# Performance work log

Hardware: AMD Instinct MI355X
Metric: run time of the kernel (lower is better)

The kernel has to match this reference:

```python
import jax, jax.numpy as jnp
import numpy as np

N_NODES = 50000
N_EDGES = 800000
IN_FEAT = 128
HIDDEN = 128
HEADS = 4
HEAD_DIM = HIDDEN // HEADS  # 32
N_LAYERS = 3
N_GRAPHS = 64
NEG_SLOPE = 0.2
LN_EPS = 1e-5


def setup_inputs() -> dict:
    key = jax.random.key(0)
    ks = jax.random.split(key, 12)
    x = jax.random.normal(ks[0], (N_NODES, IN_FEAT), dtype=jnp.float32)
    edge_index = jax.random.randint(ks[1], (2, N_EDGES), 0, N_NODES, dtype=jnp.int64)
    batch = jnp.sort(jax.random.randint(ks[2], (N_NODES,), 0, N_GRAPHS, dtype=jnp.int64))
    s = 0.05
    emb_W = jax.random.normal(ks[3], (IN_FEAT, HIDDEN), dtype=jnp.float32) * s
    emb_b = jnp.zeros((HIDDEN,), dtype=jnp.float32)
    lin_l_W = jax.random.normal(ks[4], (N_LAYERS, HIDDEN, HIDDEN), dtype=jnp.float32) * s
    lin_l_b = jnp.zeros((N_LAYERS, HIDDEN), dtype=jnp.float32)
    lin_r_W = jax.random.normal(ks[5], (N_LAYERS, HIDDEN, HIDDEN), dtype=jnp.float32) * s
    lin_r_b = jnp.zeros((N_LAYERS, HIDDEN), dtype=jnp.float32)
    att = jax.random.normal(ks[6], (N_LAYERS, HEADS, HEAD_DIM), dtype=jnp.float32) * s
    conv_b = jnp.zeros((N_LAYERS, HIDDEN), dtype=jnp.float32)
    ln_g = jnp.ones((N_LAYERS, HIDDEN), dtype=jnp.float32)
    ln_b = jnp.zeros((N_LAYERS, HIDDEN), dtype=jnp.float32)
    return {"x": x, "edge_index": edge_index, "batch": batch,
            "emb_W": emb_W, "emb_b": emb_b,
            "lin_l_W": lin_l_W, "lin_l_b": lin_l_b,
            "lin_r_W": lin_r_W, "lin_r_b": lin_r_b,
            "att": att, "conv_b": conv_b, "ln_g": ln_g, "ln_b": ln_b}


def _gatv2_layer(x, src, dst, Wl, bl, Wr, br, att_w, bias):
    # x: [N, HIDDEN]; src/dst: [E]; att_w: [H, C]
    N = x.shape[0]
    xl = (x @ Wl + bl).reshape(N, HEADS, HEAD_DIM)  # source transform
    xr = (x @ Wr + br).reshape(N, HEADS, HEAD_DIM)  # target transform
    e = jax.nn.leaky_relu(xl[src] + xr[dst], NEG_SLOPE)      # [E, H, C]
    logits = jnp.einsum('ehc,hc->eh', e, att_w)              # [E, H]
    # segment softmax over edges grouped by destination node
    seg_max = jax.ops.segment_max(logits, dst, num_segments=N)  # [N, H]
    seg_max = jnp.where(jnp.isfinite(seg_max), seg_max, 0.0)
    ex = jnp.exp(logits - seg_max[dst])
    denom = jax.ops.segment_sum(ex, dst, num_segments=N)
    alpha = ex / (denom[dst] + 1e-16)                        # [E, H]
    msg = alpha[..., None] * xl[src]                         # [E, H, C]
    out = jax.ops.segment_sum(msg, dst, num_segments=N)      # [N, H, C]
    return out.reshape(N, HIDDEN) + bias


def _layer_norm(x, g, b):
    mu = jnp.mean(x, axis=-1, keepdims=True)
    var = jnp.mean(jnp.square(x - mu), axis=-1, keepdims=True)
    return (x - mu) * jax.lax.rsqrt(var + LN_EPS) * g + b


def reference(x, edge_index, batch, emb_W, emb_b, lin_l_W, lin_l_b,
              lin_r_W, lin_r_b, att, conv_b, ln_g, ln_b):
    src, dst = edge_index[0], edge_index[1]
    h = x @ emb_W + emb_b
    for l in range(N_LAYERS):
        res = h
        h = _gatv2_layer(h, src, dst, lin_l_W[l], lin_l_b[l],
                         lin_r_W[l], lin_r_b[l], att[l], conv_b[l])
        h = jax.nn.elu(h)          # dropout in eval mode = identity
        h = h + res
        h = _layer_norm(h, ln_g[l], ln_b[l])
    # global mean pool over graphs
    sums = jax.ops.segment_sum(h, batch, num_segments=N_GRAPHS)
    counts = jax.ops.segment_sum(jnp.ones((h.shape[0], 1), h.dtype), batch,
                                 num_segments=N_GRAPHS)
    return sums / jnp.maximum(counts, 1.0)
```

## Files before the change

### kernel.cpp

```cpp
#include <hip/hip_runtime.h>
#include <hip/hip_bf16.h>
#include <math.h>


#define HID 128
#define BKT_SHIFT 7
#define BKT_DSTS (1 << BKT_SHIFT)
#define CAP_SHIFT 12
#define CAP (1 << CAP_SHIFT)

typedef __attribute__((ext_vector_type(8))) short bf8_t;
typedef __attribute__((ext_vector_type(8))) _Float16 hf8_t;
typedef __attribute__((ext_vector_type(2))) _Float16 h2_t;
typedef __attribute__((ext_vector_type(4))) float f4_t;

__device__ __forceinline__ unsigned short f2bf(float f) {
    unsigned u = __float_as_uint(f);
    u += 0x7fff + ((u >> 16) & 1);
    return (unsigned short)(u >> 16);
}
__device__ __forceinline__ float bf2f(unsigned short h) {
    return __uint_as_float(((unsigned)h) << 16);
}
__device__ __forceinline__ unsigned short f2h(float f) {
    _Float16 h = (_Float16)f;
    return __builtin_bit_cast(unsigned short, h);
}
__device__ __forceinline__ float h2f(unsigned short u) {
    return (float)__builtin_bit_cast(_Float16, u);
}
__device__ __forceinline__ h2_t shfl_xor_h2(h2_t v, int m) {
    return __builtin_bit_cast(h2_t, __shfl_xor(__builtin_bit_cast(int, v), m, 64));
}


__global__ __launch_bounds__(256) void bin_edges(const int* __restrict__ ei,
                                                 int* __restrict__ bucketCursor,
                                                 int* __restrict__ tmp,
                                                 int E, int NBK, int perBlk) {
    extern __shared__ int sh[];
    int* hist = sh;
    int* base = sh + NBK;
    int tid = threadIdx.x;
    int e0 = blockIdx.x * perBlk;
    int e1 = e0 + perBlk; if (e1 > E) e1 = E;

    for (int b = tid; b < NBK; b += 256) hist[b] = 0;
    __syncthreads();
    for (int e = e0 + tid; e < e1; e += 256)
        atomicAdd(&hist[ei[E + e] >> BKT_SHIFT], 1);
    __syncthreads();
    for (int b = tid; b < NBK; b += 256) {
        int c = hist[b];
        if (c > 0) base[b] = atomicAdd(&bucketCursor[b], c);
        hist[b] = 0;
    }
    __syncthreads();
    for (int e = e0 + tid; e < e1; e += 256) {
        int d = ei[E + e];
        int b = d >> BKT_SHIFT;
        int pos = (b << CAP_SHIFT) + base[b] + atomicAdd(&hist[b], 1);
        tmp[pos] = ei[e] | ((d & (BKT_DSTS - 1)) << 16);
    }
}

__global__ __launch_bounds__(256) void bucket_build(const int* __restrict__ tmp,
                                                    const int* __restrict__ bucketCursor,
                                                    int* __restrict__ offsets,
                                                    int* __restrict__ deg,
                                                    unsigned short* __restrict__ srt,
                                                    int N) {
    __shared__ int hist[BKT_DSTS];
    __shared__ int cur[BKT_DSTS];
    int b = blockIdx.x;
    int d0 = b << BKT_SHIFT;
    int tid = threadIdx.x;
    if (tid < BKT_DSTS) hist[tid] = 0;
    __syncthreads();
    int start = b << CAP_SHIFT;
    int end = start + bucketCursor[b];
    for (int i = start + tid; i < end; i += 256)
        atomicAdd(&hist[(tmp[i] >> 16) & (BKT_DSTS - 1)], 1);
    __syncthreads();
    int v = (tid < BKT_DSTS) ? hist[tid] : 0;
    if (tid < BKT_DSTS) cur[tid] = v;
    __syncthreads();
    for (int off = 1; off < BKT_DSTS; off <<= 1) {
        int u = (tid < BKT_DSTS && tid >= off) ? cur[tid - off] : 0;
        __syncthreads();
        if (tid < BKT_DSTS) cur[tid] += u;
        __syncthreads();
    }
    if (tid < BKT_DSTS) {
        int ex = start + cur[tid] - v;
        int d = d0 + tid;
        if (d < N) { offsets[d] = ex; deg[d] = v; }
        cur[tid] = ex;
    }
    __syncthreads();
    for (int i = start + tid; i < end; i += 256) {
        int r = tmp[i];
        int pos = atomicAdd(&cur[(r >> 16) & (BKT_DSTS - 1)], 1);
        srt[pos] = (unsigned short)(r & 0xFFFF);
    }
}

__global__ __launch_bounds__(256) void prep_wfrag_all(const float* __restrict__ embW,
                                                      const float* __restrict__ linlW,
                                                      const float* __restrict__ linrW,
                                                      unsigned short* __restrict__ frag) {
    int w = blockIdx.y;
    const float* W;
    if (w == 0)      W = embW;
    else if (w <= 3) W = linlW + (size_t)(w - 1) * 16384;
    else             W = linrW + (size_t)(w - 4) * 16384;

    int i = blockIdx.x * 256 + threadIdx.x;
    int j = i & 7;
    int lane = (i >> 3) & 63;
    int t = i >> 9;
    int kk = t >> 3, nn = t & 7;
    int k = kk * 32 + (lane >> 4) * 8 + j;
    int n = nn * 16 + (lane & 15);
    float v = W[k * 128 + n];
    if (w == 0) {
        unsigned short hi = f2bf(v);
        frag[i] = hi;
        frag[16384 + i] = f2bf(v - bf2f(hi));
    } else {
        int slot = (w <= 3) ? (1 + 2 * (w - 1)) : (2 + 2 * (w - 4));
        frag[32768 + (size_t)(slot - 1) * 16384 + i] = f2h(v);
    }
}


__global__ __launch_bounds__(256) void gemm_emb(
    const float* __restrict__ Afp,
    const unsigned short* __restrict__ Bf,
    const float* __restrict__ bias,
    unsigned short* __restrict__ Chi, unsigned short* __restrict__ Clo, int M) {
    __shared__ __align__(16) unsigned short As[2][64][136];
    int m0 = blockIdx.x * 64;
    int tid = threadIdx.x;

    #pragma unroll
    for (int i = 0; i < 8; ++i) {
        int idx = tid + i * 256;
        int r = idx >> 5, c4 = idx & 31;
        int row = m0 + r;
        float4 v = make_float4(0.f, 0.f, 0.f, 0.f);
        if (row < M) v = *(const float4*)(Afp + (size_t)row * HID + c4 * 4);
        ushort4 hi, lo;
        hi.x = f2bf(v.x); lo.x = f2bf(v.x - bf2f(hi.x));
        hi.y = f2bf(v.y); lo.y = f2bf(v.y - bf2f(hi.y));
        hi.z = f2bf(v.z); lo.z = f2bf(v.z - bf2f(hi.z));
        hi.w = f2bf(v.w); lo.w = f2bf(v.w - bf2f(hi.w));
        *(ushort4*)&As[0][r][c4 * 4] = hi;
        *(ushort4*)&As[1][r][c4 * 4] = lo;
    }
    __syncthreads();

    int wave = tid >> 6, lane = tid & 63;
    int mrow = lane & 15;
    int quad = lane >> 4;

    f4_t acc[8];
    #pragma unroll
    for (int nn = 0; nn < 8; ++nn) acc[nn] = (f4_t)(0.f);

    #pragma unroll
    for (int kk = 0; kk < 4; ++kk) {
        bf8_t ah = *(const bf8_t*)&As[0][wave * 16 + mrow][kk * 32 + quad * 8];
        bf8_t al = *(const bf8_t*)&As[1][wave * 16 + mrow][kk * 32 + quad * 8];
        const unsigned short* bp = Bf + kk * 4096 + lane * 8;
        #pragma unroll
        for (int nn = 0; nn < 8; ++nn) {
            bf8_t bh = *(const bf8_t*)(bp + nn * 512);
            bf8_t bl = *(const bf8_t*)(bp + nn * 512 + 16384);
            acc[nn] = __builtin_amdgcn_mfma_f32_16x16x32_bf16(ah, bh, acc[nn], 0, 0, 0);
            acc[nn] = __builtin_amdgcn_mfma_f32_16x16x32_bf16(ah, bl, acc[nn], 0, 0, 0);
            acc[nn] = __builtin_amdgcn_mfma_f32_16x16x32_bf16(al, bh, acc[nn], 0, 0, 0);
        }
    }

    int lrow0 = wave * 16 + quad * 4;
    __syncthreads();
    #pragma unroll
    for (int nn = 0; nn < 8; ++nn) {
        int col = nn * 16 + mrow;
        float b = bias[col];
        #pragma unroll
        for (int r = 0; r < 4; ++r) {
            float o = acc[nn][r] + b;
            unsigned short hh = f2h(o);
            As[0][lrow0 + r][col] = hh;
            As[1][lrow0 + r][col] = f2h(o - h2f(hh));
        }
    }
    __syncthreads();
    #pragma unroll
    for (int i = 0; i < 4; ++i) {
        int idx = tid + i * 256;
        int r = idx >> 4, c8 = idx & 15;
        int row = m0 + r;
        if (row < M) {
            *(uint4*)(Chi + (size_t)row * HID + c8 * 8) = *(uint4*)&As[0][r][c8 * 8];
            *(uint4*)(Clo + (size_t)row * HID + c8 * 8) = *(uint4*)&As[1][r][c8 * 8];
        }
    }
}


__global__ __launch_bounds__(256) void gemm_dual_f16(
    const unsigned short* __restrict__ Ah,
    const unsigned short* __restrict__ Bf0, const unsigned short* __restrict__ Bf1,
    const float* __restrict__ b0, const float* __restrict__ b1,
    unsigned short* __restrict__ C0h, unsigned short* __restrict__ C1h, int M) {
    __shared__ __align__(16) unsigned short As[2][64][136];
    int m0 = blockIdx.x * 64;
    int tid = threadIdx.x;

    #pragma unroll
    for (int i = 0; i < 4; ++i) {
        int idx = tid + i * 256;
        int r = idx >> 4, c8 = idx & 15;
        int row = m0 + r;
        uint4 v = make_uint4(0, 0, 0, 0);
        if (row < M) v = *(const uint4*)(Ah + (size_t)row * HID + c8 * 8);
        *(uint4*)&As[0][r][c8 * 8] = v;
    }
    __syncthreads();

    int wave = tid >> 6, lane = tid & 63;
    int mrow = lane & 15;
    int quad = lane >> 4;

    f4_t acc0[8], acc1[8];
    #pragma unroll
    for (int nn = 0; nn < 8; ++nn) {
        acc0[nn] = (f4_t)(0.f);
        acc1[nn] = (f4_t)(0.f);
    }

    #pragma unroll
    for (int kk = 0; kk < 4; ++kk) {
        hf8_t a = *(const hf8_t*)&As[0][wave * 16 + mrow][kk * 32 + quad * 8];
        const unsigned short* bp0 = Bf0 + kk * 4096 + lane * 8;
        const unsigned short* bp1 = Bf1 + kk * 4096 + lane * 8;
        #pragma unroll
        for (int nn = 0; nn < 8; ++nn) {
            hf8_t bb0 = *(const hf8_t*)(bp0 + nn * 512);
            hf8_t bb1 = *(const hf8_t*)(bp1 + nn * 512);
            acc0[nn] = __builtin_amdgcn_mfma_f32_16x16x32_f16(a, bb0, acc0[nn], 0, 0, 0);
            acc1[nn] = __builtin_amdgcn_mfma_f32_16x16x32_f16(a, bb1, acc1[nn], 0, 0, 0);
        }
    }

    int lrow0 = wave * 16 + quad * 4;
    __syncthreads();
    #pragma unroll
    for (int nn = 0; nn < 8; ++nn) {
        int col = nn * 16 + mrow;
        float bb0 = b0[col];
        float bb1 = b1[col];
        #pragma unroll
        for (int r = 0; r < 4; ++r) {
            As[0][lrow0 + r][col] = f2h(acc0[nn][r] + bb0);
            As[1][lrow0 + r][col] = f2h(acc1[nn][r] + bb1);
        }
    }
    __syncthreads();
    #pragma unroll
    for (int i = 0; i < 4; ++i) {
        int idx = tid + i * 256;
        int r = idx >> 4, c8 = idx & 15;
        int row = m0 + r;
        if (row < M) {
            *(uint4*)(C0h + (size_t)row * HID + c8 * 8) = *(uint4*)&As[0][r][c8 * 8];
            *(uint4*)(C1h + (size_t)row * HID + c8 * 8) = *(uint4*)&As[1][r][c8 * 8];
        }
    }
}


__device__ __forceinline__ void edge_math(uint4 rv, const h2_t xr2[4], const h2_t av2[4],
                                          h2_t xv[4], float* pOut) {
    const h2_t slope2 = {(_Float16)0.2f, (_Float16)0.2f};
    xv[0] = __builtin_bit_cast(h2_t, rv.x); xv[1] = __builtin_bit_cast(h2_t, rv.y);
    xv[2] = __builtin_bit_cast(h2_t, rv.z); xv[3] = __builtin_bit_cast(h2_t, rv.w);
    h2_t p2 = (h2_t)((_Float16)0.f);
    #pragma unroll
    for (int i = 0; i < 4; ++i) {
        h2_t e = xv[i] + xr2[i];
        e = __builtin_elementwise_max(e, e * slope2);
        p2 = e * av2[i] + p2;
    }
    *pOut = (float)p2[0] + (float)p2[1];
}

__global__ __launch_bounds__(256) void gat_layer(
    const unsigned short* __restrict__ xlh,
    const unsigned short* __restrict__ xrh,
    const int* __restrict__ offsets, const int* __restrict__ deg,
    const unsigned short* __restrict__ srt,
    const float* __restrict__ att,
    const float* __restrict__ convb,
    const float* __restrict__ lng, const float* __restrict__ lnb,
    unsigned short* __restrict__ Hhi, unsigned short* __restrict__ Hlo, int N) {
    int wv = (blockIdx.x * blockDim.x + threadIdx.x) >> 6;
    int lane = threadIdx.x & 63;
    if (wv >= N) return;
    int n = wv;
    int quarter = lane >> 4;
    int f0 = (lane & 15) * 8;
    const unsigned short* xbase = xlh + f0;

    h2_t xr2[4], av2[4];
    {
        uint4 xv = *(const uint4*)(xrh + (size_t)n * HID + f0);
        xr2[0] = __builtin_bit_cast(h2_t, xv.x);
        xr2[1] = __builtin_bit_cast(h2_t, xv.y);
        xr2[2] = __builtin_bit_cast(h2_t, xv.z);
        xr2[3] = __builtin_bit_cast(h2_t, xv.w);
        float a[8];
        *(float4*)&a[0] = *(const float4*)(att + f0);
        *(float4*)&a[4] = *(const float4*)(att + f0 + 4);
        #pragma unroll
        for (int i = 0; i < 4; ++i)
            av2[i] = (h2_t){(_Float16)a[2 * i], (_Float16)a[2 * i + 1]};
    }

    float d = 0.f;
    h2_t acc2[4];
    #pragma unroll
    for (int i = 0; i < 4; ++i) acc2[i] = (h2_t)((_Float16)0.f);
    int start = offsets[n], cnt = deg[n];

    int j = 0;
    for (; j + 16 <= cnt; j += 16) {
        int s[4];
        #pragma unroll
        for (int u = 0; u < 4; ++u) s[u] = srt[start + j + 4 * u + quarter];
        uint4 rv[4];
        #pragma unroll
        for (int u = 0; u < 4; ++u)
            rv[u] = *(const uint4*)(xbase + (size_t)s[u] * HID);
        h2_t xv[4][4];
        float p[4];
        #pragma unroll
        for (int u = 0; u < 4; ++u) edge_math(rv[u], xr2, av2, xv[u], &p[u]);
        h2_t p01 = {(_Float16)p[0], (_Float16)p[1]};
        h2_t p23 = {(_Float16)p[2], (_Float16)p[3]};
        p01 += shfl_xor_h2(p01, 1); p23 += shfl_xor_h2(p23, 1);
        p01 += shfl_xor_h2(p01, 2); p23 += shfl_xor_h2(p23, 2);
        float w[4];
        w[0] = __expf((float)p01[0]); w[1] = __expf((float)p01[1]);
        w[2] = __expf((float)p23[0]); w[3] = __expf((float)p23[1]);
        #pragma unroll
        for (int u = 0; u < 4; ++u) {
            d += w[u];
            h2_t w2 = (h2_t)((_Float16)w[u]);
            #pragma unroll
            for (int i = 0; i < 4; ++i) acc2[i] = w2 * xv[u][i] + acc2[i];
        }
    }
    for (; j + 4 <= cnt; j += 4) {
        int s = srt[start + j + quarter];
        uint4 rv = *(const uint4*)(xbase + (size_t)s * HID);
        h2_t xv[4];
        float p;
        edge_math(rv, xr2, av2, xv, &p);
        p += __shfl_xor(p, 1, 64);
        p += __shfl_xor(p, 2, 64);
        float w = __expf(p);
        d += w;
        h2_t w2 = (h2_t)((_Float16)w);
        #pragma unroll
        for (int i = 0; i < 4; ++i) acc2[i] = w2 * xv[i] + acc2[i];
    }
    if (j < cnt) {
        int r = cnt - j;
        int idx = j + quarter; if (idx > cnt - 1) idx = cnt - 1;
        int s = srt[start + idx];
        uint4 rv = *(const uint4*)(xbase + (size_t)s * HID);
        h2_t xv[4];
        float p;
        edge_math(rv, xr2, av2, xv, &p);
        p += __shfl_xor(p, 1, 64);
        p += __shfl_xor(p, 2, 64);
        float w = (quarter < r) ? __expf(p) : 0.f;
        d += w;
        h2_t w2 = (h2_t)((_Float16)w);
        #pragma unroll
        for (int i = 0; i < 4; ++i) acc2[i] = w2 * xv[i] + acc2[i];
    }

    #pragma unroll
    for (int i = 0; i < 4; ++i) {
        acc2[i] += shfl_xor_h2(acc2[i], 16);
        acc2[i] += shfl_xor_h2(acc2[i], 32);
    }
    d += __shfl_xor(d, 16, 64);
    d += __shfl_xor(d, 32, 64);

    float acc[8];
    #pragma unroll
    for (int i = 0; i < 4; ++i) {
        acc[2 * i]     = (float)acc2[i][0];
        acc[2 * i + 1] = (float)acc2[i][1];
    }

    float inv = 1.f / (d + 1e-16f);
    float t[8];
    {
        float cb[8];
        *(float4*)&cb[0] = *(const float4*)(convb + f0);
        *(float4*)&cb[4] = *(const float4*)(convb + f0 + 4);
        uint4 rh = *(const uint4*)(Hhi + (size_t)n * HID + f0);
        uint4 rl = *(const uint4*)(Hlo + (size_t)n * HID + f0);
        const unsigned short* hs = (const unsigned short*)&rh;
        const unsigned short* ls = (const unsigned short*)&rl;
        #pragma unroll
        for (int i = 0; i < 8; ++i) {
            float g = acc[i] * inv + cb[i];
            g = (g > 0.f) ? g : (__expf(g) - 1.f);
            t[i] = g + (h2f(hs[i]) + h2f(ls[i]));
        }
    }

    float sum = 0.f;
    #pragma unroll
    for (int i = 0; i < 8; ++i) sum += t[i];
    #pragma unroll
    for (int m = 1; m <= 8; m <<= 1) sum += __shfl_xor(sum, m, 64);
    float mu = sum * (1.f / 128.f);
    float q[8], vs = 0.f;
    #pragma unroll
    for (int i = 0; i < 8; ++i) { q[i] = t[i] - mu; vs += q[i] * q[i]; }
    #pragma unroll
    for (int m = 1; m <= 8; m <<= 1) vs += __shfl_xor(vs, m, 64);
    float rstd = rsqrtf(vs * (1.f / 128.f) + 1e-5f);

    if (quarter == 0) {
        float gv[8], bv[8], o[8];
        *(float4*)&gv[0] = *(const float4*)(lng + f0);
        *(float4*)&gv[4] = *(const float4*)(lng + f0 + 4);
        *(float4*)&bv[0] = *(const float4*)(lnb + f0);
        *(float4*)&bv[4] = *(const float4*)(lnb + f0 + 4);
        #pragma unroll
        for (int i = 0; i < 8; ++i) o[i] = q[i] * rstd * gv[i] + bv[i];
        unsigned short hh[8], hl[8];
        #pragma unroll
        for (int i = 0; i < 8; ++i) {
            hh[i] = f2h(o[i]);
            hl[i] = f2h(o[i] - h2f(hh[i]));
        }
        *(uint4*)(Hhi + (size_t)n * HID + f0) = *(uint4*)&hh[0];
        *(uint4*)(Hlo + (size_t)n * HID + f0) = *(uint4*)&hl[0];
    }
}


__global__ __launch_bounds__(256) void pool_partial(const unsigned short* __restrict__ Hhi,
                                                    const unsigned short* __restrict__ Hlo,
                                                    const int* __restrict__ batch,
                                                    float* __restrict__ sums, int N) {
    __shared__ int bsh[64];
    int c0 = blockIdx.x * 64;
    int tid = threadIdx.x;
    if (tid < 64) bsh[tid] = (c0 + tid < N) ? batch[c0 + tid] : -1;
    __syncthreads();

    int r = tid >> 5;
    int f0 = (tid & 31) * 4;
    float4 acc = make_float4(0.f, 0.f, 0.f, 0.f);
    int curg = -1;
    #pragma unroll
    for (int i = 0; i < 8; ++i) {
        int li = r * 8 + i;
        int g = bsh[li];
        if (g < 0) break;
        if (g != curg) {
            if (curg >= 0) {
                atomicAdd(&sums[curg * HID + f0 + 0], acc.x);
                atomicAdd(&sums[curg * HID + f0 + 1], acc.y);
                atomicAdd(&sums[curg * HID + f0 + 2], acc.z);
                atomicAdd(&sums[curg * HID + f0 + 3], acc.w);
            }
            acc = make_float4(0.f, 0.f, 0.f, 0.f);
            curg = g;
        }
        size_t base = (size_t)(c0 + li) * HID + f0;
        ushort4 hh = *(const ushort4*)(Hhi + base);
        ushort4 hl = *(const ushort4*)(Hlo + base);
        acc.x += h2f(hh.x) + h2f(hl.x);
        acc.y += h2f(hh.y) + h2f(hl.y);
        acc.z += h2f(hh.z) + h2f(hl.z);
        acc.w += h2f(hh.w) + h2f(hl.w);
    }
    if (curg >= 0) {
        atomicAdd(&sums[curg * HID + f0 + 0], acc.x);
        atomicAdd(&sums[curg * HID + f0 + 1], acc.y);
        atomicAdd(&sums[curg * HID + f0 + 2], acc.z);
        atomicAdd(&sums[curg * HID + f0 + 3], acc.w);
    }
}

__global__ __launch_bounds__(128) void pool_final(const float* __restrict__ sums,
                                                  const int* __restrict__ batch,
                                                  float* __restrict__ out, int N) {
    int g = blockIdx.x;
    int f = threadIdx.x;
    int lo = 0, hi = N;
    while (lo < hi) { int mid = (lo + hi) >> 1; if (batch[mid] < g) lo = mid + 1; else hi = mid; }
    int s0 = lo;
    lo = 0; hi = N;
    while (lo < hi) { int mid = (lo + hi) >> 1; if (batch[mid] < g + 1) lo = mid + 1; else hi = mid; }
    int cnt = lo - s0; if (cnt < 1) cnt = 1;
    out[g * HID + f] = sums[g * HID + f] / (float)cnt;
}


extern "C" void kernel_launch(void* const* d_in, const int* in_sizes, int n_in,
                              void* d_out, int out_size, void* d_ws, size_t ws_size,
                              hipStream_t stream) {
    const float* x      = (const float*)d_in[0];
    const int*   ei     = (const int*)d_in[1];
    const int*   batch  = (const int*)d_in[2];
    const float* emb_W  = (const float*)d_in[3];
    const float* emb_b  = (const float*)d_in[4];
    const float* linlW  = (const float*)d_in[5];
    const float* linlb  = (const float*)d_in[6];
    const float* linrW  = (const float*)d_in[7];
    const float* linrb  = (const float*)d_in[8];
    const float* att    = (const float*)d_in[9];
    const float* convb  = (const float*)d_in[10];
    const float* lng    = (const float*)d_in[11];
    const float* lnb    = (const float*)d_in[12];
    float* out = (float*)d_out;

    const int N = in_sizes[0] / HID;
    const int E = in_sizes[1] / 2;
    const int NG = out_size / HID;
    const int NBK = (N + BKT_DSTS - 1) / BKT_DSTS;

    char* p = (char*)d_ws;
    unsigned short* xlh = (unsigned short*)p; p += (size_t)N * HID * 2;
    unsigned short* xrh = (unsigned short*)p; p += (size_t)N * HID * 2;
    unsigned short* hhi = (unsigned short*)p; p += (size_t)N * HID * 2;
    unsigned short* hlo = (unsigned short*)p; p += (size_t)N * HID * 2;
    unsigned short* wfrag = (unsigned short*)p; p += (32768 + 6 * 16384) * 2;
    float* sums       = (float*)p; p += (size_t)NG * HID * 4;
    int* bucketCursor = (int*)p; p += (size_t)((NBK + 63) & ~63) * 4;
    int* deg          = (int*)p; p += (size_t)N * 4;
    int* offsets      = (int*)p; p += (size_t)N * 4;
    unsigned short* srt = (unsigned short*)p; p += ((size_t)NBK << CAP_SHIFT) * 2;
    int* tmp          = (int*)p; p += ((size_t)NBK << CAP_SHIFT) * 4;

    size_t zbytes = (size_t)NG * HID * 4 + (size_t)((NBK + 63) & ~63) * 4;
    hipMemsetAsync(sums, 0, zbytes, stream);
    {
        int nblk = 256;
        int perBlk = (E + nblk - 1) / nblk;
        bin_edges<<<nblk, 256, (size_t)2 * NBK * 4, stream>>>(ei, bucketCursor, tmp, E, NBK, perBlk);
        bucket_build<<<NBK, 256, 0, stream>>>(tmp, bucketCursor, offsets, deg, srt, N);
    }

    prep_wfrag_all<<<dim3(64, 7), 256, 0, stream>>>(emb_W, linlW, linrW, wfrag);

    int gblk = (N + 63) / 64;
    gemm_emb<<<gblk, 256, 0, stream>>>(x, wfrag, emb_b, hhi, hlo, N);

    for (int l = 0; l < 3; ++l) {
        const unsigned short* wl = wfrag + 32768 + (size_t)(2 * l) * 16384;
        const unsigned short* wr = wfrag + 32768 + (size_t)(2 * l + 1) * 16384;
        gemm_dual_f16<<<gblk, 256, 0, stream>>>(hhi, wl, wr,
                                                linlb + (size_t)l * HID,
                                                linrb + (size_t)l * HID,
                                                xlh, xrh, N);
        gat_layer<<<(N + 3) / 4, 256, 0, stream>>>(xlh, xrh, offsets, deg, srt,
                                                   att + (size_t)l * HID,
                                                   convb + (size_t)l * HID,
                                                   lng + (size_t)l * HID,
                                                   lnb + (size_t)l * HID,
                                                   hhi, hlo, N);
    }

    pool_partial<<<(N + 63) / 64, 256, 0, stream>>>(hhi, hlo, batch, sums, N);
    pool_final<<<NG, 128, 0, stream>>>(sums, batch, out, N);
}
```

Measured before the change: 347.7 us.

## Fuse edge binning with weight prep, and bucket build with embedding plus first dual GEMM

Merges bin_edges and prep_wfrag_all into one launch with disjoint block ranges. Also merges bucket_build with the embedding GEMM, and fuses the layer-0 lin_l/lin_r dual GEMM into that GEMM by reusing the fp16 hi part held in shared memory. This removes several kernel launches and one full round-trip of h through global memory for layer 0. Hist arrays are now fixed at 512 entries, which assumes NBK <= 512, and the layer-0 GEMM uses only the hi part as before.

Result: faster. 337.3 us, median of 2 (-3.0%).

```diff
diff --git a/kernel.cpp b/kernel.cpp
--- a/kernel.cpp
+++ b/kernel.cpp
@@ -34,114 +34,113 @@
 }
 
 
-__global__ __launch_bounds__(256) void bin_edges(const int* __restrict__ ei,
-                                                 int* __restrict__ bucketCursor,
-                                                 int* __restrict__ tmp,
-                                                 int E, int NBK, int perBlk) {
-    extern __shared__ int sh[];
-    int* hist = sh;
-    int* base = sh + NBK;
+__global__ __launch_bounds__(256) void k1_bin_prep(
+    const int* __restrict__ ei, int* __restrict__ bucketCursor,
+    int* __restrict__ tmp, int E, int NBK, int perBlk,
+    const float* __restrict__ embW, const float* __restrict__ linlW,
+    const float* __restrict__ linrW, unsigned short* __restrict__ frag) {
+    __shared__ int hist[512];
+    __shared__ int base[512];
     int tid = threadIdx.x;
-    int e0 = blockIdx.x * perBlk;
-    int e1 = e0 + perBlk; if (e1 > E) e1 = E;
-
-    for (int b = tid; b < NBK; b += 256) hist[b] = 0;
-    __syncthreads();
-    for (int e = e0 + tid; e < e1; e += 256)
-        atomicAdd(&hist[ei[E + e] >> BKT_SHIFT], 1);
-    __syncthreads();
-    for (int b = tid; b < NBK; b += 256) {
-        int c = hist[b];
-        if (c > 0) base[b] = atomicAdd(&bucketCursor[b], c);
-        hist[b] = 0;
-    }
-    __syncthreads();
-    for (int e = e0 + tid; e < e1; e += 256) {
-        int d = ei[E + e];
-        int b = d >> BKT_SHIFT;
-        int pos = (b << CAP_SHIFT) + base[b] + atomicAdd(&hist[b], 1);
-        tmp[pos] = ei[e] | ((d & (BKT_DSTS - 1)) << 16);
-    }
-}
-
-__global__ __launch_bounds__(256) void bucket_build(const int* __restrict__ tmp,
-                                                    const int* __restrict__ bucketCursor,
-                                                    int* __restrict__ offsets,
-                                                    int* __restrict__ deg,
-                                                    unsigned short* __restrict__ srt,
-                                                    int N) {
-    __shared__ int hist[BKT_DSTS];
-    __shared__ int cur[BKT_DSTS];
-    int b = blockIdx.x;
-    int d0 = b << BKT_SHIFT;
+
+    if (blockIdx.x < 256) {
+        int e0 = blockIdx.x * perBlk;
+        int e1 = e0 + perBlk; if (e1 > E) e1 = E;
+
+        for (int b = tid; b < NBK; b += 256) hist[b] = 0;
+        __syncthreads();
+        for (int e = e0 + tid; e < e1; e += 256)
+            atomicAdd(&hist[ei[E + e] >> BKT_SHIFT], 1);
+        __syncthreads();
+        for (int b = tid; b < NBK; b += 256) {
+            int c = hist[b];
+            if (c > 0) base[b] = atomicAdd(&bucketCursor[b], c);
+            hist[b] = 0;
+        }
+        __syncthreads();
+        for (int e = e0 + tid; e < e1; e += 256) {
+            int d = ei[E + e];
+            int b = d >> BKT_SHIFT;
+            int pos = (b << CAP_SHIFT) + base[b] + atomicAdd(&hist[b], 1);
+            tmp[pos] = ei[e] | ((d & (BKT_DSTS - 1)) << 16);
+        }
+    } else {
+        int bid = blockIdx.x - 256;
+        int w = bid >> 6;
+        const float* W;
+        if (w == 0)      W = embW;
+        else if (w <= 3) W = linlW + (size_t)(w - 1) * 16384;
+        else             W = linrW + (size_t)(w - 4) * 16384;
+
+        int i = ((bid & 63) << 8) + tid;
+        int j = i & 7;
+        int lane = (i >> 3) & 63;
+        int t = i >> 9;
+        int kk = t >> 3, nn = t & 7;
+        int k = kk * 32 + (lane >> 4) * 8 + j;
+        int n = nn * 16 + (lane & 15);
+        float v = W[k * 128 + n];
+        if (w == 0) {
+            unsigned short hi = f2bf(v);
+            frag[i] = hi;
+            frag[16384 + i] = f2bf(v - bf2f(hi));
+        } else {
+            int slot = (w <= 3) ? (1 + 2 * (w - 1)) : (2 + 2 * (w - 4));
+            frag[32768 + (size_t)(slot - 1) * 16384 + i] = f2h(v);
+        }
+    }
+}
+
+
+__global__ __launch_bounds__(256) void k2_bucket_embdual(
+    const int* __restrict__ tmp, const int* __restrict__ bucketCursor,
+    int* __restrict__ offsets, int* __restrict__ deg,
+    unsigned short* __restrict__ srt, int N, int GBLK,
+    const float* __restrict__ Afp, const unsigned short* __restrict__ wfrag,
+    const float* __restrict__ emb_b,
+    const float* __restrict__ bl0, const float* __restrict__ br0,
+    unsigned short* __restrict__ Chi, unsigned short* __restrict__ Clo,
+    unsigned short* __restrict__ xl, unsigned short* __restrict__ xr) {
+    __shared__ __align__(16) unsigned short As[2][64][136];
     int tid = threadIdx.x;
-    if (tid < BKT_DSTS) hist[tid] = 0;
-    __syncthreads();
-    int start = b << CAP_SHIFT;
-    int end = start + bucketCursor[b];
-    for (int i = start + tid; i < end; i += 256)
-        atomicAdd(&hist[(tmp[i] >> 16) & (BKT_DSTS - 1)], 1);
-    __syncthreads();
-    int v = (tid < BKT_DSTS) ? hist[tid] : 0;
-    if (tid < BKT_DSTS) cur[tid] = v;
-    __syncthreads();
-    for (int off = 1; off < BKT_DSTS; off <<= 1) {
-        int u = (tid < BKT_DSTS && tid >= off) ? cur[tid - off] : 0;
+
+    if (blockIdx.x >= GBLK) {
+        int* hist = (int*)As;
+        int* cur  = hist + BKT_DSTS;
+        int b = blockIdx.x - GBLK;
+        int d0 = b << BKT_SHIFT;
+        if (tid < BKT_DSTS) hist[tid] = 0;
         __syncthreads();
-        if (tid < BKT_DSTS) cur[tid] += u;
+        int start = b << CAP_SHIFT;
+        int end = start + bucketCursor[b];
+        for (int i = start + tid; i < end; i += 256)
+            atomicAdd(&hist[(tmp[i] >> 16) & (BKT_DSTS - 1)], 1);
         __syncthreads();
-    }
-    if (tid < BKT_DSTS) {
-        int ex = start + cur[tid] - v;
-        int d = d0 + tid;
-        if (d < N) { offsets[d] = ex; deg[d] = v; }
-        cur[tid] = ex;
-    }
-    __syncthreads();
-    for (int i = start + tid; i < end; i += 256) {
-        int r = tmp[i];
-        int pos = atomicAdd(&cur[(r >> 16) & (BKT_DSTS - 1)], 1);
-        srt[pos] = (unsigned short)(r & 0xFFFF);
-    }
-}
-
-__global__ __launch_bounds__(256) void prep_wfrag_all(const float* __restrict__ embW,
-                                                      const float* __restrict__ linlW,
-                                                      const float* __restrict__ linrW,
-                                                      unsigned short* __restrict__ frag) {
-    int w = blockIdx.y;
-    const float* W;
-    if (w == 0)      W = embW;
-    else if (w <= 3) W = linlW + (size_t)(w - 1) * 16384;
-    else             W = linrW + (size_t)(w - 4) * 16384;
-
-    int i = blockIdx.x * 256 + threadIdx.x;
-    int j = i & 7;
-    int lane = (i >> 3) & 63;
-    int t = i >> 9;
-    int kk = t >> 3, nn = t & 7;
-    int k = kk * 32 + (lane >> 4) * 8 + j;
-    int n = nn * 16 + (lane & 15);
-    float v = W[k * 128 + n];
-    if (w == 0) {
-        unsigned short hi = f2bf(v);
-        frag[i] = hi;
-        frag[16384 + i] = f2bf(v - bf2f(hi));
-    } else {
-        int slot = (w <= 3) ? (1 + 2 * (w - 1)) : (2 + 2 * (w - 4));
-        frag[32768 + (size_t)(slot - 1) * 16384 + i] = f2h(v);
-    }
-}
-
-
-__global__ __launch_bounds__(256) void gemm_emb(
-    const float* __restrict__ Afp,
-    const unsigned short* __restrict__ Bf,
-    const float* __restrict__ bias,
-    unsigned short* __restrict__ Chi, unsigned short* __restrict__ Clo, int M) {
-    __shared__ __align__(16) unsigned short As[2][64][136];
+        int v = (tid < BKT_DSTS) ? hist[tid] : 0;
+        if (tid < BKT_DSTS) cur[tid] = v;
+        __syncthreads();
+        for (int off = 1; off < BKT_DSTS; off <<= 1) {
+            int u = (tid < BKT_DSTS && tid >= off) ? cur[tid - off] : 0;
+            __syncthreads();
+            if (tid < BKT_DSTS) cur[tid] += u;
+            __syncthreads();
+        }
+        if (tid < BKT_DSTS) {
+            int ex = start + cur[tid] - v;
+            int d = d0 + tid;
+            if (d < N) { offsets[d] = ex; deg[d] = v; }
+            cur[tid] = ex;
+        }
+        __syncthreads();
+        for (int i = start + tid; i < end; i += 256) {
+            int r = tmp[i];
+            int pos = atomicAdd(&cur[(r >> 16) & (BKT_DSTS - 1)], 1);
+            srt[pos] = (unsigned short)(r & 0xFFFF);
+        }
+        return;
+    }
+
     int m0 = blockIdx.x * 64;
-    int tid = threadIdx.x;
 
     #pragma unroll
     for (int i = 0; i < 8; ++i) {
@@ -149,7 +148,7 @@
         int r = idx >> 5, c4 = idx & 31;
         int row = m0 + r;
         float4 v = make_float4(0.f, 0.f, 0.f, 0.f);
-        if (row < M) v = *(const float4*)(Afp + (size_t)row * HID + c4 * 4);
+        if (row < N) v = *(const float4*)(Afp + (size_t)row * HID + c4 * 4);
         ushort4 hi, lo;
         hi.x = f2bf(v.x); lo.x = f2bf(v.x - bf2f(hi.x));
         hi.y = f2bf(v.y); lo.y = f2bf(v.y - bf2f(hi.y));
@@ -172,7 +171,7 @@
     for (int kk = 0; kk < 4; ++kk) {
         bf8_t ah = *(const bf8_t*)&As[0][wave * 16 + mrow][kk * 32 + quad * 8];
         bf8_t al = *(const bf8_t*)&As[1][wave * 16 + mrow][kk * 32 + quad * 8];
-        const unsigned short* bp = Bf + kk * 4096 + lane * 8;
+        const unsigned short* bp = wfrag + kk * 4096 + lane * 8;
         #pragma unroll
         for (int nn = 0; nn < 8; ++nn) {
             bf8_t bh = *(const bf8_t*)(bp + nn * 512);
@@ -188,7 +187,7 @@
     #pragma unroll
     for (int nn = 0; nn < 8; ++nn) {
         int col = nn * 16 + mrow;
-        float b = bias[col];
+        float b = emb_b[col];
         #pragma unroll
         for (int r = 0; r < 4; ++r) {
             float o = acc[nn][r] + b;
@@ -198,14 +197,64 @@
         }
     }
     __syncthreads();
+
+    hf8_t afr[4];
+    #pragma unroll
+    for (int kk = 0; kk < 4; ++kk)
+        afr[kk] = *(const hf8_t*)&As[0][wave * 16 + mrow][kk * 32 + quad * 8];
     #pragma unroll
     for (int i = 0; i < 4; ++i) {
         int idx = tid + i * 256;
         int r = idx >> 4, c8 = idx & 15;
         int row = m0 + r;
-        if (row < M) {
+        if (row < N) {
             *(uint4*)(Chi + (size_t)row * HID + c8 * 8) = *(uint4*)&As[0][r][c8 * 8];
             *(uint4*)(Clo + (size_t)row * HID + c8 * 8) = *(uint4*)&As[1][r][c8 * 8];
+        }
+    }
+
+    f4_t acc0[8], acc1[8];
+    #pragma unroll
+    for (int nn = 0; nn < 8; ++nn) {
+        acc0[nn] = (f4_t)(0.f);
+        acc1[nn] = (f4_t)(0.f);
+    }
+    const unsigned short* Bl = wfrag + 32768;
+    const unsigned short* Br = wfrag + 49152;
+    #pragma unroll
+    for (int kk = 0; kk < 4; ++kk) {
+        const unsigned short* bp0 = Bl + kk * 4096 + lane * 8;
+        const unsigned short* bp1 = Br + kk * 4096 + lane * 8;
+        #pragma unroll
+        for (int nn = 0; nn < 8; ++nn) {
+            hf8_t bb0 = *(const hf8_t*)(bp0 + nn * 512);
+            hf8_t bb1 = *(const hf8_t*)(bp1 + nn * 512);
+            acc0[nn] = __builtin_amdgcn_mfma_f32_16x16x32_f16(afr[kk], bb0, acc0[nn], 0, 0, 0);
+            acc1[nn] = __builtin_amdgcn_mfma_f32_16x16x32_f16(afr[kk], bb1, acc1[nn], 0, 0, 0);
+        }
+    }
+
+    __syncthreads();
+    #pragma unroll
+    for (int nn = 0; nn < 8; ++nn) {
+        int col = nn * 16 + mrow;
+        float bb0 = bl0[col];
+        float bb1 = br0[col];
+        #pragma unroll
+        for (int r = 0; r < 4; ++r) {
+            As[0][lrow0 + r][col] = f2h(acc0[nn][r] + bb0);
+            As[1][lrow0 + r][col] = f2h(acc1[nn][r] + bb1);
+        }
+    }
+    __syncthreads();
+    #pragma unroll
+    for (int i = 0; i < 4; ++i) {
+        int idx = tid + i * 256;
+        int r = idx >> 4, c8 = idx & 15;
+        int row = m0 + r;
+        if (row < N) {
+            *(uint4*)(xl + (size_t)row * HID + c8 * 8) = *(uint4*)&As[0][r][c8 * 8];
+            *(uint4*)(xr + (size_t)row * HID + c8 * 8) = *(uint4*)&As[1][r][c8 * 8];
         }
     }
 }
@@ -559,19 +608,21 @@
 
     size_t zbytes = (size_t)NG * HID * 4 + (size_t)((NBK + 63) & ~63) * 4;
     hipMemsetAsync(sums, 0, zbytes, stream);
-    {
-        int nblk = 256;
-        int perBlk = (E + nblk - 1) / nblk;
-        bin_edges<<<nblk, 256, (size_t)2 * NBK * 4, stream>>>(ei, bucketCursor, tmp, E, NBK, perBlk);
-        bucket_build<<<NBK, 256, 0, stream>>>(tmp, bucketCursor, offsets, deg, srt, N);
-    }
-
-    prep_wfrag_all<<<dim3(64, 7), 256, 0, stream>>>(emb_W, linlW, linrW, wfrag);
+
+    int perBlk = (E + 255) / 256;
+    k1_bin_prep<<<256 + 448, 256, 0, stream>>>(ei, bucketCursor, tmp, E, NBK, perBlk,
+                                               emb_W, linlW, linrW, wfrag);
 
     int gblk = (N + 63) / 64;
-    gemm_emb<<<gblk, 256, 0, stream>>>(x, wfrag, emb_b, hhi, hlo, N);
-
-    for (int l = 0; l < 3; ++l) {
+    k2_bucket_embdual<<<gblk + NBK, 256, 0, stream>>>(tmp, bucketCursor, offsets, deg,
+                                                      srt, N, gblk,
+                                                      x, wfrag, emb_b, linlb, linrb,
+                                                      hhi, hlo, xlh, xrh);
+
+    gat_layer<<<(N + 3) / 4, 256, 0, stream>>>(xlh, xrh, offsets, deg, srt,
+                                               att, convb, lng, lnb, hhi, hlo, N);
+
+    for (int l = 1; l < 3; ++l) {
         const unsigned short* wl = wfrag + 32768 + (size_t)(2 * l) * 16384;
         const unsigned short* wr = wfrag + 32768 + (size_t)(2 * l + 1) * 16384;
         gemm_dual_f16<<<gblk, 256, 0, stream>>>(hhi, wl, wr,
```
